# Performance work log

Measured on AMD Instinct MI355X. Metric: run time of the kernel, lower is better.

## Reference

```python
import jax, jax.numpy as jnp
import numpy as np

N_BINS = ((1, 1), (2, 2), (4, 4), (8, 8))  # SPP pyramid; sum(ph*pw) = 85


def _pool_one_scale(x, ph, pw):
    """Max-pool x [B,H,W,C] into ph x pw bins.

    Bin i covers rows [i*hs, (i+1)*hs) except the last, which extends to H
    (matching the TF layer's floor-step + last-bin-extends semantics).
    Returns [B, ph*pw*C] flattened in (bin_i, bin_j, channel) order.
    """
    B, H, W, C = x.shape
    hs, ws = H // ph, W // pw
    # pool over height
    main = x[:, : (ph - 1) * hs].reshape(B, ph - 1, hs, W, C).max(axis=2)
    last = x[:, (ph - 1) * hs :].max(axis=1, keepdims=True)
    xh = jnp.concatenate([main, last], axis=1)  # [B, ph, W, C]
    # pool over width
    main = xh[:, :, : (pw - 1) * ws].reshape(B, ph, pw - 1, ws, C).max(axis=3)
    last = xh[:, :, (pw - 1) * ws :].max(axis=2, keepdims=True)
    out = jnp.concatenate([main, last], axis=2)  # [B, ph, pw, C]
    return out.reshape(B, ph * pw * C)


def setup_inputs() -> dict:
    key = jax.random.key(0)
    x = jax.random.normal(key, (32, 64, 64, 512), dtype=jnp.float32)
    return {"x": x}


def reference(x):
    # concat multi-scale pooled embeddings -> [B, sum(ph*pw)*C]
    return jnp.concatenate([_pool_one_scale(x, ph, pw) for ph, pw in N_BINS], axis=1)
```

## Files before the change

### kernel.cpp

```cpp
#include <hip/hip_runtime.h>
#include <hip/hip_bf16.h>
#include <math.h>


#define C_F4 128
#define ROW_OUT 43520
#define S8_OFF 10752
#define S4_OFF 2560
#define S2_OFF 512

typedef float vf4 __attribute__((ext_vector_type(4)));

static __device__ __forceinline__ vf4 vmax(vf4 a, vf4 b) {
    vf4 r;
    r.x = fmaxf(a.x, b.x);
    r.y = fmaxf(a.y, b.y);
    r.z = fmaxf(a.z, b.z);
    r.w = fmaxf(a.w, b.w);
    return r;
}

__global__ __launch_bounds__(256) void spp_pool84(const float* __restrict__ x,
                                                  float* __restrict__ out) {
    const int blk = blockIdx.x;
    const int b   = blk >> 4;
    const int rem = blk & 15;
    const int i4  = rem >> 2;
    const int j4  = rem & 3;
    const int tid = threadIdx.x;
    const int s   = tid >> 7;
    const int c4  = tid & 127;

    const int row0 = i4 * 16 + s * 8;
    const vf4* src = reinterpret_cast<const vf4*>(x)
                   + (size_t)((b * 64 + row0) * 64 + j4 * 16) * C_F4 + c4;

    vf4 m0 = __builtin_nontemporal_load(src);
    vf4 m1 = __builtin_nontemporal_load(src + 8 * 128);
    #pragma unroll 2
    for (int h = 0; h < 8; ++h) {
        #pragma unroll
        for (int w = 0; w < 8; ++w) {
            if (h == 0 && w == 0) continue;
            m0 = vmax(m0, __builtin_nontemporal_load(src + h * 8192 + w * 128));
            m1 = vmax(m1, __builtin_nontemporal_load(src + h * 8192 + (w + 8) * 128));
        }
    }

    float* row = out + (size_t)b * ROW_OUT;
    const int i8 = 2 * i4 + s;
    const int j8 = 2 * j4;
    __builtin_nontemporal_store(m0, reinterpret_cast<vf4*>(row + S8_OFF + (i8 * 8 + j8) * 512) + c4);
    __builtin_nontemporal_store(m1, reinterpret_cast<vf4*>(row + S8_OFF + (i8 * 8 + j8 + 1) * 512) + c4);

    __shared__ vf4 ls[2][128];
    ls[s][c4] = vmax(m0, m1);
    __syncthreads();
    if (s == 0) {
        vf4 v4 = vmax(ls[0][c4], ls[1][c4]);
        reinterpret_cast<vf4*>(row + S4_OFF + (i4 * 4 + j4) * 512)[c4] = v4;
    }
}

__global__ __launch_bounds__(512) void spp_tail(float* __restrict__ out) {
    const int b   = blockIdx.x;
    const int tid = threadIdx.x;
    const int q   = tid >> 7;
    const int c4  = tid & 127;
    const int i2  = q >> 1;
    const int j2  = q & 1;

    float* row = out + (size_t)b * ROW_OUT;
    const vf4* p4 = reinterpret_cast<const vf4*>(row + S4_OFF) + c4;

    vf4 m =     p4[((2 * i2)     * 4 + 2 * j2)     * C_F4];
    m = vmax(m, p4[((2 * i2)     * 4 + 2 * j2 + 1) * C_F4]);
    m = vmax(m, p4[((2 * i2 + 1) * 4 + 2 * j2)     * C_F4]);
    m = vmax(m, p4[((2 * i2 + 1) * 4 + 2 * j2 + 1) * C_F4]);

    reinterpret_cast<vf4*>(row + S2_OFF + q * 512)[c4] = m;

    __shared__ vf4 ls[4][128];
    ls[q][c4] = m;
    __syncthreads();
    if (q == 0) {
        vf4 v1 = vmax(vmax(ls[0][c4], ls[1][c4]),
                      vmax(ls[2][c4], ls[3][c4]));
        reinterpret_cast<vf4*>(row)[c4] = v1;
    }
}

extern "C" void kernel_launch(void* const* d_in, const int* in_sizes, int n_in,
                              void* d_out, int out_size, void* d_ws, size_t ws_size,
                              hipStream_t stream) {
    const float* x = (const float*)d_in[0];
    float* out = (float*)d_out;

    spp_pool84<<<512, 256, 0, stream>>>(x, out);
    spp_tail<<<32, 512, 0, stream>>>(out);
}
```

Before: 47.72 us.

## Split channels across blocks and shorten per-thread row chains for more parallelism

The pooling kernel now launches twice as many blocks, with each block covering half the channels and each thread reducing 4 rows instead of 8. Partial maxima are combined through shared memory into the 8x8 and 4x4 bins. Loads switch from nontemporal to normal loads and the loop is fully unrolled. The aim is more blocks and more loads in flight to saturate memory bandwidth on a 256-CU part, at the cost of an extra shared-memory reduction step and a second barrier.

```diff
diff --git a/kernel.cpp b/kernel.cpp
--- a/kernel.cpp
+++ b/kernel.cpp
@@ -23,42 +23,54 @@
 __global__ __launch_bounds__(256) void spp_pool84(const float* __restrict__ x,
                                                   float* __restrict__ out) {
     const int blk = blockIdx.x;
-    const int b   = blk >> 4;
-    const int rem = blk & 15;
-    const int i4  = rem >> 2;
-    const int j4  = rem & 3;
+    const int b     = blk >> 5;
+    const int rem   = blk & 31;
+    const int i4    = rem >> 3;
+    const int j4    = (rem >> 1) & 3;
+    const int chalf = rem & 1;
     const int tid = threadIdx.x;
-    const int s   = tid >> 7;
-    const int c4  = tid & 127;
+    const int s   = tid >> 6;
+    const int c4i = tid & 63;
+    const int c4g = chalf * 64 + c4i;
 
-    const int row0 = i4 * 16 + s * 8;
+    const int row0 = i4 * 16 + s * 4;
     const vf4* src = reinterpret_cast<const vf4*>(x)
-                   + (size_t)((b * 64 + row0) * 64 + j4 * 16) * C_F4 + c4;
+                   + (size_t)((b * 64 + row0) * 64 + j4 * 16) * C_F4 + c4g;
 
-    vf4 m0 = __builtin_nontemporal_load(src);
-    vf4 m1 = __builtin_nontemporal_load(src + 8 * 128);
-    #pragma unroll 2
-    for (int h = 0; h < 8; ++h) {
+    vf4 m0 = src[0];
+    vf4 m1 = src[8 * 128];
+    #pragma unroll
+    for (int h = 0; h < 4; ++h) {
         #pragma unroll
         for (int w = 0; w < 8; ++w) {
             if (h == 0 && w == 0) continue;
-            m0 = vmax(m0, __builtin_nontemporal_load(src + h * 8192 + w * 128));
-            m1 = vmax(m1, __builtin_nontemporal_load(src + h * 8192 + (w + 8) * 128));
+            m0 = vmax(m0, src[h * 8192 + w * 128]);
+            m1 = vmax(m1, src[h * 8192 + (w + 8) * 128]);
         }
     }
 
+    __shared__ vf4 ls0[4][64];
+    __shared__ vf4 ls1[4][64];
+    ls0[s][c4i] = m0;
+    ls1[s][c4i] = m1;
+    __syncthreads();
+
     float* row = out + (size_t)b * ROW_OUT;
-    const int i8 = 2 * i4 + s;
-    const int j8 = 2 * j4;
-    __builtin_nontemporal_store(m0, reinterpret_cast<vf4*>(row + S8_OFF + (i8 * 8 + j8) * 512) + c4);
-    __builtin_nontemporal_store(m1, reinterpret_cast<vf4*>(row + S8_OFF + (i8 * 8 + j8 + 1) * 512) + c4);
-
-    __shared__ vf4 ls[2][128];
-    ls[s][c4] = vmax(m0, m1);
+    if (s < 2) {
+        const int i8 = 2 * i4 + s;
+        const int j8 = 2 * j4;
+        vf4 bin0 = vmax(ls0[2 * s][c4i], ls0[2 * s + 1][c4i]);
+        vf4 bin1 = vmax(ls1[2 * s][c4i], ls1[2 * s + 1][c4i]);
+        __builtin_nontemporal_store(bin0,
+            reinterpret_cast<vf4*>(row + S8_OFF + (i8 * 8 + j8) * 512) + c4g);
+        __builtin_nontemporal_store(bin1,
+            reinterpret_cast<vf4*>(row + S8_OFF + (i8 * 8 + j8 + 1) * 512) + c4g);
+        ls0[s][c4i] = vmax(bin0, bin1);
+    }
     __syncthreads();
     if (s == 0) {
-        vf4 v4 = vmax(ls[0][c4], ls[1][c4]);
-        reinterpret_cast<vf4*>(row + S4_OFF + (i4 * 4 + j4) * 512)[c4] = v4;
+        vf4 v4 = vmax(ls0[0][c4i], ls0[1][c4i]);
+        reinterpret_cast<vf4*>(row + S4_OFF + (i4 * 4 + j4) * 512)[c4g] = v4;
     }
 }
 
@@ -96,6 +108,6 @@
     const float* x = (const float*)d_in[0];
     float* out = (float*)d_out;
 
-    spp_pool84<<<512, 256, 0, stream>>>(x, out);
+    spp_pool84<<<1024, 256, 0, stream>>>(x, out);
     spp_tail<<<32, 512, 0, stream>>>(out);
 }
```

Result: faster. 46.11 us (-3.4%).
